# Kernel optimization log

Measured on AMD Instinct MI355X. Metric: run time of the kernel, lower is better.

Reference implementation:

```python
import jax, jax.numpy as jnp
import numpy as np

L = 4        # num_layers
H = 1024     # hidden_size
NH = 16      # num_heads
KVH = 4      # num_kv_heads
QPK = NH // KVH
HD = H // NH # head_dim = 64
FF = 4096    # intermediate_size
V = 32000    # vocab_size
B, S = 2, 2048
EPS = 1e-5
STD = 0.02


def layernorm(x, g, b):
    m = jnp.mean(x, axis=-1, keepdims=True)
    v = jnp.mean(jnp.square(x - m), axis=-1, keepdims=True)
    return (x - m) * jax.lax.rsqrt(v + EPS) * g + b


def setup_inputs() -> dict:
    key = jax.random.key(0)
    ks = iter(jax.random.split(key, 24))
    n = lambda shape: STD * jax.random.normal(next(ks), shape, dtype=jnp.float32)
    KV = H * KVH // NH  # kv_size = 256
    inp = {
        'input_ids': jax.random.randint(next(ks), (B, S), 0, V),
        'attention_mask': jnp.zeros((B, S), dtype=jnp.float32),
        'tok_emb': n((V, H)),
        'pos_emb': n((S, H)),
        # per-layer stacked weights, stored [in, out] so y = x @ W + b
        'Wq': n((L, H, H)),  'bq': jnp.zeros((L, H)),
        'Wk': n((L, H, KV)), 'bk': jnp.zeros((L, KV)),
        'Wv': n((L, H, KV)), 'bv': jnp.zeros((L, KV)),
        'Wo': n((L, H, H)),  'bo': jnp.zeros((L, H)),
        'W1': n((L, H, FF)), 'b1': jnp.zeros((L, FF)),
        'W2': n((L, FF, H)), 'b2': jnp.zeros((L, H)),
        'ln1_g': jnp.ones((L, H)), 'ln1_b': jnp.zeros((L, H)),
        'ln2_g': jnp.ones((L, H)), 'ln2_b': jnp.zeros((L, H)),
        'lnf_g': jnp.ones((H,)),   'lnf_b': jnp.zeros((H,)),
        'Whead': n((H, V)),  # head has no bias
    }
    return inp


def gpt_forward(input_ids, attention_mask, tok_emb, pos_emb,
                Wq, bq, Wk, bk, Wv, bv, Wo, bo,
                W1, b1, W2, b2, ln1_g, ln1_b, ln2_g, ln2_b,
                lnf_g, lnf_b, Whead):
    b, s = input_ids.shape
    x = tok_emb[input_ids] + pos_emb[None, :s, :]  # [b,s,H]
    mask = attention_mask[:, None, None, None, :]  # [b,1,1,1,s] additive
    scale = 1.0 / jnp.sqrt(jnp.float32(HD))
    for l in range(L):
        h = layernorm(x, ln1_g[l], ln1_b[l])
        q = h @ Wq[l] + bq[l]                              # [b,s,H]
        k = h @ Wk[l] + bk[l]                              # [b,s,KV]
        v = h @ Wv[l] + bv[l]
        q = q.reshape(b, s, KVH, QPK, HD).transpose(0, 2, 3, 1, 4)  # [b,g,q,s,d]
        k = k.reshape(b, s, KVH, HD).transpose(0, 2, 1, 3)          # [b,g,s,d]
        v = v.reshape(b, s, KVH, HD).transpose(0, 2, 1, 3)
        scores = jnp.einsum('bgqsd,bgkd->bgqsk', q, k) * scale      # [b,g,q,s,s]
        scores = scores + mask
        w = jax.nn.softmax(scores, axis=-1)
        o = jnp.einsum('bgqsk,bgkd->bgqsd', w, v)                   # [b,g,q,s,d]
        o = o.transpose(0, 3, 1, 2, 4).reshape(b, s, H)
        x = x + (o @ Wo[l] + bo[l])
        h2 = layernorm(x, ln2_g[l], ln2_b[l])
        ff = jax.nn.gelu(h2 @ W1[l] + b1[l], approximate=False) @ W2[l] + b2[l]
        x = x + ff
    x = layernorm(x, lnf_g, lnf_b)
    return x @ Whead  # [b,s,V] logits


def reference(input_ids, attention_mask, tok_emb, pos_emb,
              Wq, bq, Wk, bk, Wv, bv, Wo, bo,
              W1, b1, W2, b2, ln1_g, ln1_b, ln2_g, ln2_b,
              lnf_g, lnf_b, Whead):
    return gpt_forward(input_ids, attention_mask, tok_emb, pos_emb,
                       Wq, bq, Wk, bk, Wv, bv, Wo, bo,
                       W1, b1, W2, b2, ln1_g, ln1_b, ln2_g, ln2_b,
                       lnf_g, lnf_b, Whead)
```

## Files before the change

kernel.cpp:

```cpp
#include <hip/hip_runtime.h>
#include <hip/hip_bf16.h>

#define LAYERS 4
#define H 1024
#define NH 16
#define KVH 4
#define HD 64
#define KVD 256
#define FF 4096
#define VOC 32000
#define BB 2
#define SS 2048
#define MROWS (BB*SS)
#define QKVN 1536

typedef __attribute__((ext_vector_type(4))) float f32x4;
typedef __attribute__((ext_vector_type(8))) short short8;
typedef __attribute__((ext_vector_type(4))) unsigned short u16x4;
typedef __attribute__((ext_vector_type(2))) unsigned int u32x2;

__device__ inline unsigned short f2bf(float f){
  union { float f; unsigned u; } v; v.f = f;
  return (unsigned short)((v.u + 0x7FFFu + ((v.u >> 16) & 1u)) >> 16);
}
__device__ inline unsigned cvt_pk_bf16(float a, float b){
  unsigned r;
  asm("v_cvt_pk_bf16_f32 %0, %1, %2" : "=v"(r) : "v"(a), "v"(b));
  return r;
}

__global__ __launch_bounds__(256) void embed_kernel(const int* __restrict__ ids,
    const float* __restrict__ tok, const float* __restrict__ pos, float* __restrict__ x)
{
  int row = blockIdx.x;
  int s = row & (SS-1);
  int id = ids[row];
  int t = threadIdx.x;
  f32x4 a = *(const f32x4*)&tok[(size_t)id*H + t*4];
  f32x4 p = *(const f32x4*)&pos[(size_t)s*H + t*4];
  *(f32x4*)&x[(size_t)row*H + t*4] = a + p;
}

__global__ __launch_bounds__(256) void ln_kernel(const float* __restrict__ x,
    const float* __restrict__ g, const float* __restrict__ b, unsigned short* __restrict__ out)
{
  int row = blockIdx.x;
  int t = threadIdx.x;
  const float* xr = x + (size_t)row*H;
  f32x4 v = *(const f32x4*)&xr[t*4];
  float s  = v[0]+v[1]+v[2]+v[3];
  float s2 = v[0]*v[0]+v[1]*v[1]+v[2]*v[2]+v[3]*v[3];
  #pragma unroll
  for (int off=1; off<64; off<<=1){ s += __shfl_xor(s,off); s2 += __shfl_xor(s2,off); }
  __shared__ float red[8];
  int w = t>>6;
  if ((t&63)==0){ red[w]=s; red[4+w]=s2; }
  __syncthreads();
  float S1 = red[0]+red[1]+red[2]+red[3];
  float S2 = red[4]+red[5]+red[6]+red[7];
  float mean = S1 * (1.0f/H);
  float var  = S2 * (1.0f/H) - mean*mean;
  float rs = rsqrtf(var + 1e-5f);
  u16x4 o;
  #pragma unroll
  for (int i=0;i<4;i++) o[i] = f2bf((v[i]-mean)*rs*g[t*4+i] + b[t*4+i]);
  *(u16x4*)&out[(size_t)row*H + t*4] = o;
}

__global__ __launch_bounds__(256) void convT_kernel(const float* __restrict__ in,
    unsigned short* __restrict__ out, int K, int N, size_t istride, size_t ostride)
{
  __shared__ float t[32][33];
  in  += (size_t)blockIdx.z * istride;
  out += (size_t)blockIdx.z * ostride;
  int n0 = blockIdx.x*32, k0 = blockIdx.y*32;
  int x = threadIdx.x & 31, y = threadIdx.x >> 5;
  #pragma unroll
  for (int j=0;j<4;j++) t[y+j*8][x] = in[(size_t)(k0+y+j*8)*N + n0 + x];
  __syncthreads();
  int x2 = threadIdx.x & 15, y2 = threadIdx.x >> 4;
  #pragma unroll
  for (int j=0;j<2;j++){
    int n = y2 + j*16;
    unsigned lo = f2bf(t[x2*2][n]);
    unsigned hi = f2bf(t[x2*2+1][n]);
    *(unsigned*)&out[(size_t)(n0+n)*K + k0 + x2*2] = lo | (hi<<16);
  }
}

__global__ __launch_bounds__(256) void bcat_kernel(const float* __restrict__ bq,
    const float* __restrict__ bk, const float* __restrict__ bv, float* __restrict__ out)
{
  int l = blockIdx.x, t = threadIdx.x;
  #pragma unroll
  for (int i=0;i<4;i++) out[l*QKVN + t + i*256] = bq[l*H + t + i*256];
  out[l*QKVN + 1024 + t] = bk[l*KVD + t];
  out[l*QKVN + 1280 + t] = bv[l*KVD + t];
}

template<int EPI>
__global__ __launch_bounds__(256, 2) void gemm_bt(
    const unsigned short* __restrict__ A, const unsigned short* __restrict__ Bt,
    const float* __restrict__ bias, const float* __restrict__ res,
    float* __restrict__ outf, unsigned short* __restrict__ outb,
    unsigned short* __restrict__ outb2, unsigned short* __restrict__ outb3, int N, int K)
{
  __shared__ __align__(16) char lds[65536];
  const int tid = threadIdx.x;
  const int lane = tid & 63, wid = tid >> 6;
  const int wr = (wid>>1)*64, wc = (wid&1)*64;
  const int fr = lane & 15, fq = lane >> 4;
  const int m0 = blockIdx.x*128, n0 = blockIdx.y*128;
  const int nt = K >> 5;
  f32x4 acc[4][4] = {};

  #define STG1(PTR, baserow, kt, ldsoff) do {                                   \
    _Pragma("unroll")                                                           \
    for (int c=0;c<2;c++){                                                      \
      int rr = c*64 + (tid>>2);                                                 \
      int ss = (tid&3) ^ ((rr>>1)&3);                                           \
      __builtin_amdgcn_global_load_lds(                                         \
        (const __attribute__((address_space(1))) void*)((PTR) + (size_t)((baserow)+rr)*K + (kt)*32 + ss*8), \
        (__attribute__((address_space(3))) void*)(lds + (ldsoff) + c*4096 + wid*1024), 16, 0, 0); \
    }                                                                           \
  } while(0)
  #define RDA1(buf,row) (*(const short8*)(lds + (buf)*16384 + (row)*64 + ((fq ^ (((row)>>1)&3))*16)))
  #define RDB1(buf,row) (*(const short8*)(lds + (buf)*16384 + 8192 + (row)*64 + ((fq ^ (((row)>>1)&3))*16)))

  STG1(A,  m0, 0, 0);      STG1(Bt, n0, 0, 8192);
  STG1(A,  m0, 1, 16384);  STG1(Bt, n0, 1, 16384+8192);
  STG1(A,  m0, 2, 32768);  STG1(Bt, n0, 2, 32768+8192);
  asm volatile("s_waitcnt vmcnt(8)" ::: "memory");
  __builtin_amdgcn_s_barrier();

  for (int t = 0; t < nt; ++t){
    const int buf = t & 3;
    const int s3 = (t+3) & 3;
    const int t3 = (t+3 < nt) ? t+3 : t;
    short8 af[4], bf[4];
    #pragma unroll
    for (int mi=0;mi<4;mi++) af[mi] = RDA1(buf, wr+mi*16+fr);
    #pragma unroll
    for (int ni=0;ni<4;ni++) bf[ni] = RDB1(buf, wc+ni*16+fr);
    STG1(A,  m0, t3, s3*16384);
    STG1(Bt, n0, t3, s3*16384+8192);
    __builtin_amdgcn_s_barrier();
    asm volatile("s_waitcnt lgkmcnt(0)" ::: "memory");
    __builtin_amdgcn_s_setprio(1);
    #pragma unroll
    for (int mi=0;mi<4;mi++)
      #pragma unroll
      for (int ni=0;ni<4;ni++)
        acc[mi][ni] = __builtin_amdgcn_mfma_f32_16x16x32_bf16(af[mi], bf[ni], acc[mi][ni], 0,0,0);
    __builtin_amdgcn_s_setprio(0);
    asm volatile("s_waitcnt vmcnt(8)" ::: "memory");
    __builtin_amdgcn_s_barrier();
  }
  #undef STG1
  #undef RDA1
  #undef RDB1

  #pragma unroll
  for (int mi=0;mi<4;mi++)
    #pragma unroll
    for (int ni=0;ni<4;ni++){
      int col = n0 + wc + ni*16 + fr;
      float bi = (EPI==3) ? 0.0f : bias[col];
      #pragma unroll
      for (int r=0;r<4;r++){
        int row = m0 + wr + mi*16 + fq*4 + r;
        float vv = acc[mi][ni][r] + bi;
        if (EPI==1)      { size_t idx=(size_t)row*N+col; outf[idx] = vv + res[idx]; }
        else if (EPI==2) { size_t idx=(size_t)row*N+col; outb[idx] = f2bf(0.5f*vv*(1.0f+erff(vv*0.70710678118f))); }
        else if (EPI==3) { size_t idx=(size_t)row*N+col; outf[idx] = vv; }
        else if (EPI==5) {
          if (col < 1024)      outb [(size_t)row*H + col]            = f2bf(vv);
          else if (col < 1280) outb2[(size_t)row*KVD + (col-1024)]   = f2bf(vv);
          else                 outb3[(size_t)(col-1280)*MROWS + row] = f2bf(vv);
        }
      }
    }
}

template<int EPI>
__global__ __launch_bounds__(512, 2) void gemm256(
    const unsigned short* __restrict__ A, const unsigned short* __restrict__ Bt,
    const float* __restrict__ bias, float* __restrict__ outf,
    unsigned short* __restrict__ outb, int N, int K)
{
  __shared__ __align__(16) char lds[131072];
  const int tid = threadIdx.x;
  const int lane = tid & 63, wid = tid >> 6;
  const int wrr = wid >> 2, wc = wid & 3;
  const int fr = lane & 15, fq = lane >> 4;
  const int m0 = blockIdx.x*256, n0 = blockIdx.y*256;
  const int nt = K >> 5;
  f32x4 acc[8][4] = {};

  #define STG(PTR, baserow, kt, ldsoff) do {                                    \
    _Pragma("unroll")                                                           \
    for (int c=0;c<2;c++){                                                      \
      int rr = c*128 + (tid>>2);                                                \
      int ss = (tid&3) ^ ((rr>>1)&3);                                           \
      __builtin_amdgcn_global_load_lds(                                         \
        (const __attribute__((address_space(1))) void*)((PTR) + (size_t)((baserow)+rr)*K + (kt)*32 + ss*8), \
        (__attribute__((address_space(3))) void*)(lds + (ldsoff) + c*8192 + wid*1024), 16, 0, 0); \
    }                                                                           \
  } while(0)
  #define RDA(buf,row) (*(const short8*)(lds + (buf)*32768 + (row)*64 + ((fq ^ (((row)>>1)&3))*16)))
  #define RDB(buf,row) (*(const short8*)(lds + (buf)*32768 + 16384 + (row)*64 + ((fq ^ (((row)>>1)&3))*16)))

  STG(A,  m0, 0, 0);      STG(Bt, n0, 0, 16384);
  STG(A,  m0, 1, 32768);  STG(Bt, n0, 1, 32768+16384);
  STG(A,  m0, 2, 65536);  STG(Bt, n0, 2, 65536+16384);
  asm volatile("s_waitcnt vmcnt(8)" ::: "memory");
  __builtin_amdgcn_s_barrier();

  for (int t = 0; t < nt; ++t){
    const int buf = t & 3;
    const int s3 = (t+3) & 3;
    const int t3 = (t+3 < nt) ? t+3 : t;
    short8 bf[4], af[8];
    #pragma unroll
    for (int ni=0;ni<4;ni++) bf[ni] = RDB(buf, wc*64+ni*16+fr);
    #pragma unroll
    for (int mi=0;mi<8;mi++) af[mi] = RDA(buf, wrr*128+mi*16+fr);
    STG(A,  m0, t3, s3*32768);
    STG(Bt, n0, t3, s3*32768+16384);
    __builtin_amdgcn_s_barrier();
    asm volatile("s_waitcnt lgkmcnt(0)" ::: "memory");
    __builtin_amdgcn_s_setprio(1);
    #pragma unroll
    for (int mi=0;mi<8;mi++)
      #pragma unroll
      for (int ni=0;ni<4;ni++)
        acc[mi][ni] = __builtin_amdgcn_mfma_f32_16x16x32_bf16(af[mi], bf[ni], acc[mi][ni], 0,0,0);
    __builtin_amdgcn_s_setprio(0);
    asm volatile("s_waitcnt vmcnt(8)" ::: "memory");
    __builtin_amdgcn_s_barrier();
  }
  #undef STG
  #undef RDA
  #undef RDB

  #pragma unroll
  for (int mi=0; mi<8; mi++)
    #pragma unroll
    for (int ni=0; ni<4; ni++){
      int col = n0 + wc*64 + ni*16 + fr;
      float bi = (EPI==3) ? 0.0f : bias[col];
      #pragma unroll
      for (int r=0; r<4; r++){
        int row = m0 + wrr*128 + mi*16 + fq*4 + r;
        float vv = acc[mi][ni][r] + bi;
        size_t idx = (size_t)row*N + col;
        if (EPI==3) outf[idx] = vv;
        else        outb[idx] = f2bf(0.5f*vv*(1.0f+erff(vv*0.70710678118f)));
      }
    }
}

#define LOG2E 1.4426950408889634f
__global__ __launch_bounds__(256) void attn_kernel(
    const unsigned short* __restrict__ q, const unsigned short* __restrict__ kptr,
    const unsigned short* __restrict__ vt, const float* __restrict__ mask,
    unsigned short* __restrict__ o)
{
  __shared__ char Pbuf[4][4096];
  int tid = threadIdx.x;
  int lane = tid & 63, wid = tid >> 6;
  int fr = lane & 15, fq = lane >> 4, fo = fq*8;
  int h = blockIdx.y, b = blockIdx.z, g = h >> 2;
  int qcol = h*HD, kcol = g*HD;
  int qbase = b*SS + blockIdx.x*128 + wid*32;
  char* Pl = Pbuf[wid];
  int swz = (fr & 7) << 4;

  short8 bq[2][2];
  #pragma unroll
  for (int h2=0; h2<2; h2++){
    const unsigned short* qrow = q + (size_t)(qbase + h2*16 + fr)*H + qcol;
    bq[h2][0] = *(const short8*)(qrow + fo);
    bq[h2][1] = *(const short8*)(qrow + 32 + fo);
  }

  f32x4 oacc[2][4] = {};
  float mrun[2] = {-1e30f, -1e30f}, lsum[2] = {0.f, 0.f};
  const float sc2 = 0.125f * LOG2E;

  const unsigned short* kp[4];
  #pragma unroll
  for (int f=0; f<4; f++) kp[f] = kptr + (size_t)(b*SS + f*16 + fr)*KVD + kcol + fo;
  const unsigned short* vp[4];
  #pragma unroll
  for (int dc=0; dc<4; dc++) vp[dc] = vt + (size_t)(kcol + dc*16 + fr)*MROWS + b*SS + fo;
  const float* mp = mask + b*SS + fq*4;

  short8 kaA[4][2], kaB[4][2];
  #pragma unroll
  for (int f=0; f<4; f++){
    kaA[f][0] = *(const short8*)(kp[f]);
    kaA[f][1] = *(const short8*)(kp[f] + 32);
    kp[f] += 64*KVD;
  }

#define ATTN_STEP(KA, KB, PF) do {                                             \
    f32x4 mkv[4];                                                              \
    _Pragma("unroll")                                                          \
    for (int f=0; f<4; f++) mkv[f] = *(const f32x4*)(mp + f*16);               \
    short8 va[4][2];                                                           \
    _Pragma("unroll")                                                          \
    for (int dc=0; dc<4; dc++){                                                \
      va[dc][0] = *(const short8*)(vp[dc]);                                    \
      va[dc][1] = *(const short8*)(vp[dc] + 32);                               \
    }                                                                          \
    f32x4 sf[2][4] = {};                                                       \
    __builtin_amdgcn_s_setprio(1);                                             \
    _Pragma("unroll")                                                          \
    for (int h2=0; h2<2; h2++)                                                 \
      _Pragma("unroll")                                                        \
      for (int f=0; f<4; f++){                                                 \
        sf[h2][f] = __builtin_amdgcn_mfma_f32_16x16x32_bf16(KA[f][0], bq[h2][0], sf[h2][f],0,0,0); \
        sf[h2][f] = __builtin_amdgcn_mfma_f32_16x16x32_bf16(KA[f][1], bq[h2][1], sf[h2][f],0,0,0); \
      }                                                                        \
    __builtin_amdgcn_s_setprio(0);                                             \
    if (PF){                                                                   \
      _Pragma("unroll")                                                        \
      for (int f=0; f<4; f++){                                                 \
        KB[f][0] = *(const short8*)(kp[f]);                                    \
        KB[f][1] = *(const short8*)(kp[f] + 32);                               \
        kp[f] += 64*KVD;                                                       \
      }                                                                        \
    }                                                                          \
    _Pragma("unroll")                                                          \
    for (int f=0; f<4; f++){                                                   \
      _Pragma("unroll")                                                        \
      for (int r=0; r<4; r++){                                                 \
        float m2 = mkv[f][r]*LOG2E;                                            \
        sf[0][f][r] = sf[0][f][r]*sc2 + m2;                                    \
        sf[1][f][r] = sf[1][f][r]*sc2 + m2;                                    \
      }                                                                        \
    }                                                                          \
    float pm[2];                                                               \
    _Pragma("unroll")                                                          \
    for (int h2=0; h2<2; h2++){                                                \
      float a0 = fmaxf(fmaxf(sf[h2][0][0],sf[h2][0][1]), fmaxf(sf[h2][0][2],sf[h2][0][3])); \
      float a1 = fmaxf(fmaxf(sf[h2][1][0],sf[h2][1][1]), fmaxf(sf[h2][1][2],sf[h2][1][3])); \
      float a2 = fmaxf(fmaxf(sf[h2][2][0],sf[h2][2][1]), fmaxf(sf[h2][2][2],sf[h2][2][3])); \
      float a3 = fmaxf(fmaxf(sf[h2][3][0],sf[h2][3][1]), fmaxf(sf[h2][3][2],sf[h2][3][3])); \
      float p = fmaxf(fmaxf(a0,a1), fmaxf(a2,a3));                             \
      p = fmaxf(p, __shfl_xor(p, 16));                                         \
      p = fmaxf(p, __shfl_xor(p, 32));                                         \
      pm[h2] = p;                                                              \
    }                                                                          \
    if (!__all(pm[0] <= mrun[0]+8.f && pm[1] <= mrun[1]+8.f)){                 \
      float al[2];                                                             \
      _Pragma("unroll")                                                        \
      for (int h2=0; h2<2; h2++){                                              \
        float mn = fmaxf(mrun[h2], pm[h2]);                                    \
        al[h2] = __builtin_amdgcn_exp2f(mrun[h2]-mn);                          \
        mrun[h2] = mn;                                                         \
        lsum[h2] *= al[h2];                                                    \
      }                                                                        \
      _Pragma("unroll")                                                        \
      for (int r=0; r<4; r++){                                                 \
        float altl = __shfl(al[0], fq*4+r);                                    \
        float alth = __shfl(al[1], fq*4+r);                                    \
        _Pragma("unroll")                                                      \
        for (int dc=0; dc<4; dc++){ oacc[0][dc][r]*=altl; oacc[1][dc][r]*=alth; } \
      }                                                                        \
    }                                                                          \
    _Pragma("unroll")                                                          \
    for (int h2=0; h2<2; h2++){                                                \
      float ps = 0.f;                                                          \
      _Pragma("unroll")                                                        \
      for (int f=0; f<4; f++)                                                  \
        _Pragma("unroll")                                                      \
        for (int r=0; r<4; r++){                                               \
          float e = __builtin_amdgcn_exp2f(sf[h2][f][r]-mrun[h2]);             \
          sf[h2][f][r] = e; ps += e;                                           \
        }                                                                      \
      ps += __shfl_xor(ps, 16);                                                \
      ps += __shfl_xor(ps, 32);                                                \
      lsum[h2] += ps;                                                          \
    }                                                                          \
    _Pragma("unroll")                                                          \
    for (int h2=0; h2<2; h2++){                                                \
      int prow = h2*16 + fr;                                                   \
      _Pragma("unroll")                                                        \
      for (int f=0; f<4; f++){                                                 \
        u32x2 pw;                                                              \
        pw[0] = cvt_pk_bf16(sf[h2][f][0], sf[h2][f][1]);                       \
        pw[1] = cvt_pk_bf16(sf[h2][f][2], sf[h2][f][3]);                       \
        *(u32x2*)(Pl + prow*128 + ((f*32 + fq*8) ^ swz)) = pw;                 \
      }                                                                        \
    }                                                                          \
    __builtin_amdgcn_s_setprio(1);                                             \
    _Pragma("unroll")                                                          \
    for (int h2=0; h2<2; h2++){                                                \
      int prow = h2*16 + fr;                                                   \
      _Pragma("unroll")                                                        \
      for (int gs=0; gs<2; gs++){                                              \
        short8 pa = *(const short8*)(Pl + prow*128 + ((gs*64 + fq*16) ^ swz)); \
        _Pragma("unroll")                                                      \
        for (int dc=0; dc<4; dc++)                                             \
          oacc[h2][dc] = __builtin_amdgcn_mfma_f32_16x16x32_bf16(pa, va[dc][gs], oacc[h2][dc],0,0,0); \
      }                                                                        \
    }                                                                          \
    __builtin_amdgcn_s_setprio(0);                                             \
    _Pragma("unroll")                                                          \
    for (int dc=0; dc<4; dc++) vp[dc] += 64;                                   \
    mp += 64;                                                                  \
  } while(0)

  for (int it = 0; it < SS/128 - 1; ++it){
    ATTN_STEP(kaA, kaB, 1);
    ATTN_STEP(kaB, kaA, 1);
  }
  ATTN_STEP(kaA, kaB, 1);
  ATTN_STEP(kaB, kaA, 0);
#undef ATTN_STEP

  #pragma unroll
  for (int h2=0; h2<2; h2++){
    float lt[4];
    #pragma unroll
    for (int r=0; r<4; r++) lt[r] = __shfl(lsum[h2], fq*4+r);
    #pragma unroll
    for (int dc=0; dc<4; dc++)
      #pragma unroll
      for (int r=0; r<4; r++){
        int row = qbase + h2*16 + fq*4 + r;
        o[(size_t)row*H + qcol + dc*16 + fr] = f2bf(oacc[h2][dc][r] / lt[r]);
      }
  }
}

extern "C" void kernel_launch(void* const* d_in, const int* in_sizes, int n_in,
                              void* d_out, int out_size, void* d_ws, size_t ws_size,
                              hipStream_t stream)
{
  const int*   ids  = (const int*)  d_in[0];
  const float* mask = (const float*)d_in[1];
  const float* tok  = (const float*)d_in[2];
  const float* pos  = (const float*)d_in[3];
  const float* Wq   = (const float*)d_in[4];
  const float* bq   = (const float*)d_in[5];
  const float* Wk   = (const float*)d_in[6];
  const float* bk   = (const float*)d_in[7];
  const float* Wv   = (const float*)d_in[8];
  const float* bv   = (const float*)d_in[9];
  const float* Wo   = (const float*)d_in[10];
  const float* bo   = (const float*)d_in[11];
  const float* W1   = (const float*)d_in[12];
  const float* b1   = (const float*)d_in[13];
  const float* W2   = (const float*)d_in[14];
  const float* b2   = (const float*)d_in[15];
  const float* ln1g = (const float*)d_in[16];
  const float* ln1b = (const float*)d_in[17];
  const float* ln2g = (const float*)d_in[18];
  const float* ln2b = (const float*)d_in[19];
  const float* lnfg = (const float*)d_in[20];
  const float* lnfb = (const float*)d_in[21];
  const float* Wh   = (const float*)d_in[22];
  float* out = (float*)d_out;

  char* ws = (char*)d_ws;
  float*          x    = (float*)ws;          ws += (size_t)MROWS*H*4;
  unsigned short* hb   = (unsigned short*)ws; ws += (size_t)MROWS*H*2;
  unsigned short* qb   = (unsigned short*)ws; ws += (size_t)MROWS*H*2;
  unsigned short* kb   = (unsigned short*)ws; ws += (size_t)MROWS*KVD*2;
  unsigned short* vtb  = (unsigned short*)ws; ws += (size_t)KVD*MROWS*2;
  unsigned short* ob   = (unsigned short*)ws; ws += (size_t)MROWS*H*2;
  unsigned short* f1   = (unsigned short*)ws; ws += (size_t)MROWS*FF*2;
  unsigned short* Wqkv = (unsigned short*)ws; ws += (size_t)LAYERS*QKVN*H*2;
  unsigned short* WoT  = (unsigned short*)ws; ws += (size_t)LAYERS*H*H*2;
  unsigned short* W1T  = (unsigned short*)ws; ws += (size_t)LAYERS*H*FF*2;
  unsigned short* W2T  = (unsigned short*)ws; ws += (size_t)LAYERS*H*FF*2;
  unsigned short* WhT  = (unsigned short*)ws; ws += (size_t)H*VOC*2;
  float*          bcat = (float*)ws;          ws += (size_t)LAYERS*QKVN*4;

  convT_kernel<<<dim3(H/32,   H/32,  LAYERS), 256, 0, stream>>>(Wq, Wqkv,          H,  H,   (size_t)H*H,   (size_t)QKVN*H);
  convT_kernel<<<dim3(KVD/32, H/32,  LAYERS), 256, 0, stream>>>(Wk, Wqkv + 1024*H, H,  KVD, (size_t)H*KVD, (size_t)QKVN*H);
  convT_kernel<<<dim3(KVD/32, H/32,  LAYERS), 256, 0, stream>>>(Wv, Wqkv + 1280*H, H,  KVD, (size_t)H*KVD, (size_t)QKVN*H);
  convT_kernel<<<dim3(H/32,   H/32,  LAYERS), 256, 0, stream>>>(Wo, WoT,           H,  H,   (size_t)H*H,   (size_t)H*H);
  convT_kernel<<<dim3(FF/32,  H/32,  LAYERS), 256, 0, stream>>>(W1, W1T,           H,  FF,  (size_t)H*FF,  (size_t)H*FF);
  convT_kernel<<<dim3(H/32,   FF/32, LAYERS), 256, 0, stream>>>(W2, W2T,           FF, H,   (size_t)FF*H,  (size_t)FF*H);
  convT_kernel<<<dim3(VOC/32, H/32,  1),      256, 0, stream>>>(Wh, WhT,           H,  VOC, 0, 0);
  bcat_kernel<<<LAYERS, 256, 0, stream>>>(bq, bk, bv, bcat);

  embed_kernel<<<MROWS, 256, 0, stream>>>(ids, tok, pos, x);
  for (int l=0; l<LAYERS; l++){
    ln_kernel<<<MROWS,256,0,stream>>>(x, ln1g + l*H, ln1b + l*H, hb);
    gemm_bt<5><<<dim3(MROWS/128, QKVN/128),256,0,stream>>>(hb, Wqkv + (size_t)l*QKVN*H, bcat + l*QKVN, nullptr, nullptr, qb, kb, vtb, QKVN, H);
    attn_kernel<<<dim3(SS/128, NH, BB), 256, 0, stream>>>(qb, kb, vtb, mask, ob);
    gemm_bt<1><<<dim3(MROWS/128, H/128),  256,0,stream>>>(ob, WoT + (size_t)l*H*H,  bo + l*H,  x, x, nullptr, nullptr, nullptr, H, H);
    ln_kernel<<<MROWS,256,0,stream>>>(x, ln2g + l*H, ln2b + l*H, hb);
    gemm256<2><<<dim3(MROWS/256, FF/256), 512,0,stream>>>(hb, W1T + (size_t)l*H*FF, b1 + l*FF, nullptr, f1, FF, H);
    gemm_bt<1><<<dim3(MROWS/128, H/128),  256,0,stream>>>(f1, W2T + (size_t)l*H*FF, b2 + l*H,  x, x, nullptr, nullptr, nullptr, H, FF);
  }
  ln_kernel<<<MROWS,256,0,stream>>>(x, lnfg, lnfb, hb);
  gemm256<3><<<dim3(MROWS/256, VOC/256), 512,0,stream>>>(hb, WhT, nullptr, out, nullptr, VOC, H);
}
```

Baseline: 1.696 ms.

## Software-pipeline LDS fragment reads with MFMA in GEMM main loop

Restructures the GEMM k-loop so part of the A and B fragments for the next tile are read from LDS after the barrier and overlap with the remaining MFMAs of the current tile. The MFMA block is split into four quarters, interleaved with the global-to-LDS staging issues. This drops one barrier per iteration and is meant to hide LDS read latency behind matrix math. It raises register pressure from the extra live fragments, and the clamp for the last tile changes to nt-1.

```diff
diff --git a/kernel.cpp b/kernel.cpp
--- a/kernel.cpp
+++ b/kernel.cpp
@@ -216,28 +216,63 @@
   asm volatile("s_waitcnt vmcnt(8)" ::: "memory");
   __builtin_amdgcn_s_barrier();
 
+  short8 a[4], b2[2];
+  short8 bA = RDB(0, wc*64+fr);
+  short8 bB = RDB(0, wc*64+16+fr);
+  #pragma unroll
+  for (int mi=0;mi<4;mi++) a[mi] = RDA(0, wrr*128+mi*16+fr);
+
   for (int t = 0; t < nt; ++t){
     const int buf = t & 3;
     const int s3 = (t+3) & 3;
-    const int t3 = (t+3 < nt) ? t+3 : t;
-    short8 bf[4], af[8];
-    #pragma unroll
-    for (int ni=0;ni<4;ni++) bf[ni] = RDB(buf, wc*64+ni*16+fr);
-    #pragma unroll
-    for (int mi=0;mi<8;mi++) af[mi] = RDA(buf, wrr*128+mi*16+fr);
-    STG(A,  m0, t3, s3*32768);
+    const int nb = (t+1) & 3;
+    const int t3 = (t+3 < nt) ? t+3 : nt-1;
+    short8 ah[4];
+    #pragma unroll
+    for (int mi=0;mi<4;mi++) ah[mi] = RDA(buf, wrr*128+(4+mi)*16+fr);
+    b2[0] = RDB(buf, wc*64+32+fr);
+    b2[1] = RDB(buf, wc*64+48+fr);
+    STG(A, m0, t3, s3*32768);
+    __builtin_amdgcn_s_setprio(1);
+    #pragma unroll
+    for (int mi=0;mi<4;mi++){
+      acc[mi][0] = __builtin_amdgcn_mfma_f32_16x16x32_bf16(a[mi], bA, acc[mi][0], 0,0,0);
+      acc[mi][1] = __builtin_amdgcn_mfma_f32_16x16x32_bf16(a[mi], bB, acc[mi][1], 0,0,0);
+    }
+    __builtin_amdgcn_s_setprio(0);
     STG(Bt, n0, t3, s3*32768+16384);
-    __builtin_amdgcn_s_barrier();
+    __builtin_amdgcn_s_setprio(1);
+    #pragma unroll
+    for (int mi=0;mi<4;mi++){
+      acc[4+mi][0] = __builtin_amdgcn_mfma_f32_16x16x32_bf16(ah[mi], bA, acc[4+mi][0], 0,0,0);
+      acc[4+mi][1] = __builtin_amdgcn_mfma_f32_16x16x32_bf16(ah[mi], bB, acc[4+mi][1], 0,0,0);
+    }
+    __builtin_amdgcn_s_setprio(0);
     asm volatile("s_waitcnt lgkmcnt(0)" ::: "memory");
-    __builtin_amdgcn_s_setprio(1);
-    #pragma unroll
-    for (int mi=0;mi<8;mi++)
-      #pragma unroll
-      for (int ni=0;ni<4;ni++)
-        acc[mi][ni] = __builtin_amdgcn_mfma_f32_16x16x32_bf16(af[mi], bf[ni], acc[mi][ni], 0,0,0);
-    __builtin_amdgcn_s_setprio(0);
     asm volatile("s_waitcnt vmcnt(8)" ::: "memory");
     __builtin_amdgcn_s_barrier();
+    short8 nbA = RDB(nb, wc*64+fr);
+    short8 nbB = RDB(nb, wc*64+16+fr);
+    short8 na[4];
+    #pragma unroll
+    for (int mi=0;mi<4;mi++) na[mi] = RDA(nb, wrr*128+mi*16+fr);
+    __builtin_amdgcn_s_setprio(1);
+    #pragma unroll
+    for (int mi=0;mi<4;mi++){
+      acc[mi][2] = __builtin_amdgcn_mfma_f32_16x16x32_bf16(a[mi], b2[0], acc[mi][2], 0,0,0);
+      acc[mi][3] = __builtin_amdgcn_mfma_f32_16x16x32_bf16(a[mi], b2[1], acc[mi][3], 0,0,0);
+    }
+    __builtin_amdgcn_s_setprio(0);
+    __builtin_amdgcn_s_setprio(1);
+    #pragma unroll
+    for (int mi=0;mi<4;mi++){
+      acc[4+mi][2] = __builtin_amdgcn_mfma_f32_16x16x32_bf16(ah[mi], b2[0], acc[4+mi][2], 0,0,0);
+      acc[4+mi][3] = __builtin_amdgcn_mfma_f32_16x16x32_bf16(ah[mi], b2[1], acc[4+mi][3], 0,0,0);
+    }
+    __builtin_amdgcn_s_setprio(0);
+    bA = nbA; bB = nbB;
+    #pragma unroll
+    for (int mi=0;mi<4;mi++) a[mi] = na[mi];
   }
   #undef STG
   #undef RDA
```

Measured after the change: 1.665 ms. Within noise of the previous version (-1.8%).
